# Kernel optimization log

Hardware: AMD Instinct MI355X
Metric: run time of the kernel (lower is better)

## Reference

```python
import jax, jax.numpy as jnp
import numpy as np

DIM = 256        # word / relation / entity-type embedding dim
STATEDIM = 256   # agent state dim
VOCAB = 100000
REL_COUNT = 25
T = 128          # sentence length


def _lstm(wvs, Wih, Whh, bih, bhh, reverse):
    # PyTorch LSTMCell gate order: i, f, g, o
    def step(carry, x):
        h, c = carry
        g = x @ Wih.T + bih + h @ Whh.T + bhh
        i, f, gg, o = jnp.split(g, 4)
        c = jax.nn.sigmoid(f) * c + jax.nn.sigmoid(i) * jnp.tanh(gg)
        h = jax.nn.sigmoid(o) * jnp.tanh(c)
        return (h, c), h
    init = (jnp.zeros((DIM,), jnp.float32), jnp.zeros((DIM,), jnp.float32))
    _, hs = jax.lax.scan(step, init, wvs, reverse=reverse)
    return hs


def setup_inputs() -> dict:
    key = jax.random.key(0)
    ks = jax.random.split(key, 32)
    def p(i, shape, scale=0.05):
        return (jax.random.normal(ks[i], shape) * scale).astype(jnp.float32)
    return {
        "text": jax.random.randint(ks[0], (T,), 0, VOCAB, dtype=jnp.int32),
        "wordvector": p(1, (VOCAB, DIM)),
        "relvec": p(2, (REL_COUNT + 1, DIM)),
        "entvec": p(3, (7, DIM)),
        "WihL": p(4, (4 * DIM, DIM)), "WhhL": p(5, (4 * DIM, DIM)),
        "bihL": p(6, (4 * DIM,)), "bhhL": p(7, (4 * DIM,)),
        "WihR": p(8, (4 * DIM, DIM)), "WhhR": p(9, (4 * DIM, DIM)),
        "bihR": p(10, (4 * DIM,)), "bhhR": p(11, (4 * DIM,)),
        "Wt": p(12, (STATEDIM, 3 * DIM + STATEDIM)), "bt": p(13, (STATEDIM,)),
        "Wp": p(14, (REL_COUNT + 1, STATEDIM)), "bp": p(15, (REL_COUNT + 1,)),
        "Wb": p(16, (STATEDIM, 3 * DIM + 2 * STATEDIM)), "bb": p(17, (STATEDIM,)),
        "Wpl": p(18, (REL_COUNT, 7, STATEDIM)), "bpl": p(19, (REL_COUNT, 7)),
        "Wtt": p(20, (STATEDIM, STATEDIM)), "btt": p(21, (STATEDIM,)),
        "Wtb": p(22, (STATEDIM, STATEDIM)), "btb": p(23, (STATEDIM,)),
        "Wbt": p(24, (STATEDIM, STATEDIM)), "bbt": p(25, (STATEDIM,)),
    }


def reference(text, wordvector, relvec, entvec, WihL, WhhL, bihL, bhhL,
              WihR, WhhR, bihR, bhhR, Wt, bt, Wp, bp, Wb, bb, Wpl, bpl,
              Wtt, btt, Wtb, btb, Wbt, bbt):
    # mode = "test_NER": deterministic argmax sampling, dropout disabled.
    wvs = wordvector[text]                               # [T, DIM]
    front = _lstm(wvs, WihL, WhhL, bihL, bhhL, False)    # [T, DIM]
    back = _lstm(wvs, WihR, WhhR, bihR, bhhR, True)      # [T, DIM]
    wordin = jnp.concatenate([front, back], axis=1)      # [T, 2*DIM]

    def bot_rollout(rel_idx, target, memb0):
        Wr, br = Wpl[rel_idx], bpl[rel_idx]              # per-relation head
        def stepb(carry, w):
            memb, ab = carry
            inpb = jnp.concatenate([w, entvec[ab], memb, target])
            outb = jnp.tanh(inpb @ Wb.T + bb)            # dropout off (test)
            probb = jax.nn.softmax(outb @ Wr.T + br)
            ab2 = jnp.argmax(probb).astype(jnp.int32)
            return (outb, ab2), (ab2, probb[ab2])
        (membf, _), (acts, aps) = jax.lax.scan(
            stepb, (memb0, jnp.zeros((), jnp.int32)), wordin)
        return membf, acts, aps

    def top_step(carry, w):
        mem, rel_action = carry
        inp = jnp.concatenate([w, relvec[rel_action], mem])
        outp = jnp.tanh(inp @ Wt.T + bt)                 # dropout off (test)
        prob = jax.nn.softmax(outp @ Wp.T + bp)
        action = jnp.argmax(prob).astype(jnp.int32)
        actprob = prob[action]
        do_ner = action > 0
        rel_next = jnp.where(do_ner, action, rel_action)
        rel_idx = jnp.maximum(action, 1) - 1
        target = outp @ Wtt.T + btt
        memb0 = outp @ Wtb.T + btb
        membf, acts, aps = bot_rollout(rel_idx, target, memb0)
        mem_after = membf @ Wbt.T + bbt
        mem_next = jnp.where(do_ner, mem_after, outp)
        acts = jnp.where(do_ner, acts, 0)
        aps = jnp.where(do_ner, aps, 0.0)
        return (mem_next, rel_next), (action, actprob, acts, aps)

    init = (jnp.zeros((STATEDIM,), jnp.float32), jnp.zeros((), jnp.int32))
    _, (top_actions, top_actprobs, bot_actions, bot_actprobs) = jax.lax.scan(
        top_step, init, wordin)
    # bot rows where no NER sub-rollout fired are zero-filled (orig: empty lists)
    return top_actions, top_actprobs, bot_actions, bot_actprobs
```

## Files before the change

kernel.cpp:

```cpp
#include <hip/hip_runtime.h>
#include <float.h>

constexpr int SEQ  = 128;
constexpr int D    = 256;
constexpr int G    = 1024;
constexpr int NREL = 26;
constexpr int NENT = 7;

typedef float v2f __attribute__((ext_vector_type(2)));

__global__ void k_trans(const float* __restrict__ in, float* __restrict__ out,
                        int rows, int cols, int in_stride, int in_off)
{
    int idx = blockIdx.x * 256 + threadIdx.x;
    if (idx >= rows * cols) return;
    int i = idx % rows;
    int k = idx / rows;
    out[idx] = in[(size_t)i * in_stride + in_off + k];
}

__global__ __launch_bounds__(1024) void k_xg(
    const int* __restrict__ text, const float* __restrict__ wv,
    const float* __restrict__ Wih, const float* __restrict__ bih,
    const float* __restrict__ bhh, float* __restrict__ xg)
{
    int t = blockIdx.x, j = threadIdx.x;
    const float* x  = wv + (size_t)text[t] * D;
    const float* wr = Wih + (size_t)j * D;
    float acc = bih[j] + bhh[j];
    for (int k = 0; k < D; ++k) acc += x[k] * wr[k];
    xg[t * G + j] = acc;
}

__global__ __launch_bounds__(1024) void k_lstm(
    const float* __restrict__ xgF, const float* __restrict__ xgB,
    const float* __restrict__ WHTF, const float* __restrict__ WHTB,
    float* __restrict__ wordin)
{
    int dir = blockIdx.x;
    const float* xg  = dir ? xgB  : xgF;
    const float* WHT = dir ? WHTB : WHTF;
    __shared__ float h[D], c[D], g[G];
    int j = threadIdx.x;
    if (j < D) { h[j] = 0.f; c[j] = 0.f; }
    __syncthreads();
    for (int s = 0; s < SEQ; ++s) {
        int t = dir ? (SEQ - 1 - s) : s;
        float acc = xg[t * G + j];
        for (int k = 0; k < D; ++k) acc += WHT[k * G + j] * h[k];
        g[j] = acc;
        __syncthreads();
        if (j < D) {
            float si = 1.f / (1.f + expf(-g[j]));
            float sf = 1.f / (1.f + expf(-g[D + j]));
            float gg = tanhf(g[2 * D + j]);
            float so = 1.f / (1.f + expf(-g[3 * D + j]));
            float cn = sf * c[j] + si * gg;
            float hn = so * tanhf(cn);
            c[j] = cn; h[j] = hn;
            wordin[t * (2 * D) + dir * D + j] = hn;
        }
        __syncthreads();
    }
}

__global__ __launch_bounds__(256) void k_prep2(
    const float* __restrict__ wordin,
    const float* __restrict__ WTWT, const float* __restrict__ WBWT,
    const float* __restrict__ WTRT, const float* __restrict__ WBET,
    const float* __restrict__ relvec, const float* __restrict__ entvec,
    const float* __restrict__ btv, const float* __restrict__ bbv,
    float* __restrict__ TW, float* __restrict__ BW,
    float* __restrict__ RV, float* __restrict__ EV)
{
    int b = blockIdx.x, i = threadIdx.x;
    if (b < SEQ) {
        const float* w = wordin + b * (2 * D);
        float a1 = btv[i], a2 = bbv[i];
        for (int j = 0; j < 2 * D; ++j) {
            float wv = w[j];
            a1 += wv * WTWT[j * D + i];
            a2 += wv * WBWT[j * D + i];
        }
        TW[b * D + i] = a1;
        BW[b * D + i] = a2;
    } else if (b < SEQ + NREL) {
        int r = b - SEQ;
        const float* x = relvec + r * D;
        float a = 0.f;
        for (int k = 0; k < D; ++k) a += x[k] * WTRT[k * D + i];
        RV[r * D + i] = a;
    } else {
        int e = b - SEQ - NREL;
        const float* x = entvec + e * D;
        float a = 0.f;
        for (int k = 0; k < D; ++k) a += x[k] * WBET[k * D + i];
        EV[e * D + i] = a;
    }
}

__global__ __launch_bounds__(256) void k_m1(
    const float* __restrict__ WBGT, const float* __restrict__ Wtt,
    float* __restrict__ M1T)
{
    int j = blockIdx.x, i = threadIdx.x;
    float a = 0.f;
    for (int k = 0; k < D; ++k) a = fmaf(WBGT[k * D + i], Wtt[k * D + j], a);
    M1T[j * D + i] = a;
}

__global__ __launch_bounds__(256) void k_c1(
    const float* __restrict__ WBGT, const float* __restrict__ btt,
    float* __restrict__ c1)
{
    int i = threadIdx.x;
    float a = 0.f;
    for (int k = 0; k < D; ++k) a = fmaf(WBGT[k * D + i], btt[k], a);
    c1[i] = a;
}

__global__ __launch_bounds__(256) void k_pack8r(
    const float* __restrict__ Wb, float* __restrict__ WREG)
{
    int e = blockIdx.x * 256 + threadIdx.x;
    int i = e >> 7, q = e & 127;
    WREG[e] = Wb[(size_t)i * (5 * D) + 3 * D + q];
}

__global__ __launch_bounds__(256) void k_pack8l(
    const float* __restrict__ Wb, float* __restrict__ WLDS)
{
    int f = blockIdx.x * 256 + threadIdx.x;
    int f4 = f >> 2, c = f & 3;
    int l = f4 & 63, rest = f4 >> 6;
    int j = rest % 24, w = rest / 24;
    WLDS[f] = Wb[(size_t)(w * 64 + l) * (5 * D) + 3 * D + 128 + 4 * j + c];
}

__global__ __launch_bounds__(256) void k_pack8g(
    const float* __restrict__ Wb, float* __restrict__ WGL)
{
    int f = blockIdx.x * 256 + threadIdx.x;
    int f4 = f >> 2, c = f & 3;
    int i = f4 & 255, j = f4 >> 8;
    WGL[f] = Wb[(size_t)i * (5 * D) + 3 * D + 224 + 4 * j + c];
}

__device__ inline float mv_full(const float* __restrict__ Wcol,
                                const float4* __restrict__ x4)
{
    float a0 = 0.f, a1 = 0.f, a2 = 0.f, a3 = 0.f;
    #pragma unroll 8
    for (int kk = 0; kk < 64; ++kk) {
        float4 xv = x4[kk];
        a0 = fmaf(Wcol[(4 * kk + 0) * D], xv.x, a0);
        a1 = fmaf(Wcol[(4 * kk + 1) * D], xv.y, a1);
        a2 = fmaf(Wcol[(4 * kk + 2) * D], xv.z, a2);
        a3 = fmaf(Wcol[(4 * kk + 3) * D], xv.w, a3);
    }
    return (a0 + a1) + (a2 + a3);
}

template<int W>
__device__ inline void grp_smax(float lv, int n, int lane, int& am, float& pm)
{
    float mx = lv;
    #pragma unroll
    for (int off = W / 2; off; off >>= 1) mx = fmaxf(mx, __shfl_xor(mx, off));
    float e  = (lane < n) ? expf(lv - mx) : 0.f;
    float se = e;
    #pragma unroll
    for (int off = W / 2; off; off >>= 1) se += __shfl_xor(se, off);
    float p  = (lane < n) ? (e / se) : -1.f;
    float q  = p;
    #pragma unroll
    for (int off = W / 2; off; off >>= 1) q = fmaxf(q, __shfl_xor(q, off));
    unsigned long long mask = __ballot(p == q);
    am = __ffsll((long long)mask) - 1;
    pm = q;
}

#define FMA_AB(Wv, Xv)                                                        \
    { float4 xx_ = (Xv);                                                      \
      A0 = __builtin_elementwise_fma((v2f){(Wv).x, (Wv).y},                   \
                                     (v2f){xx_.x, xx_.y}, A0);                \
      A1 = __builtin_elementwise_fma((v2f){(Wv).z, (Wv).w},                   \
                                     (v2f){xx_.z, xx_.w}, A1); }
#define FMA_CD(Wv, Xv)                                                        \
    { float4 xx_ = (Xv);                                                      \
      A2 = __builtin_elementwise_fma((v2f){(Wv).x, (Wv).y},                   \
                                     (v2f){xx_.x, xx_.y}, A2);                \
      A3 = __builtin_elementwise_fma((v2f){(Wv).z, (Wv).w},                   \
                                     (v2f){xx_.z, xx_.w}, A3); }

__global__ __launch_bounds__(256)
void k_main7(
    const float* __restrict__ TW,   const float* __restrict__ BW,
    const float* __restrict__ RV,   const float* __restrict__ EV,
    const float* __restrict__ WTMT, const float* __restrict__ WTBT,
    const float* __restrict__ WBTT, const float* __restrict__ M1T,
    const float* __restrict__ c1v,  const float* __restrict__ WREG,
    const float* __restrict__ WLDS, const float* __restrict__ WGL,
    const float* __restrict__ Wp,   const float* __restrict__ bp,
    const float* __restrict__ Wpl,  const float* __restrict__ bpl,
    const float* __restrict__ btb,  const float* __restrict__ bbt,
    float* __restrict__ out)
{
    const int tid  = threadIdx.x;
    const int lane = tid & 63;
    const int w8   = tid >> 6;

    __shared__ __align__(16) float wlds[256 * 96];
    __shared__ __align__(16) float xbuf[2][D];
    __shared__ __align__(16) float mem[D], outv[D];
    __shared__ __align__(16) float Esh[NENT * D], WrSh[NENT * D];
    __shared__ float lpartT[4][32];
    __shared__ float lpartB[2][4][8];
    __shared__ float brSh[8];

    {
        const float4* g4 = reinterpret_cast<const float4*>(WLDS);
        float4* w4 = reinterpret_cast<float4*>(wlds);
        #pragma unroll
        for (int it = 0; it < 24; ++it) w4[tid + it * 256] = g4[tid + it * 256];
    }
    for (int k = tid; k < NENT * D; k += 256) Esh[k] = EV[k];
    mem[tid] = 0.f;

    const float4* r4 = reinterpret_cast<const float4*>(WREG) + tid * 32;
    float4 wr0 = r4[0],   wr1 = r4[1],   wr2 = r4[2],   wr3 = r4[3];
    float4 wr4 = r4[4],   wr5 = r4[5],   wr6 = r4[6],   wr7 = r4[7];
    float4 wr8 = r4[8],   wr9 = r4[9],   wr10 = r4[10], wr11 = r4[11];
    float4 wr12 = r4[12], wr13 = r4[13], wr14 = r4[14], wr15 = r4[15];
    float4 wr16 = r4[16], wr17 = r4[17], wr18 = r4[18], wr19 = r4[19];
    float4 wr20 = r4[20], wr21 = r4[21], wr22 = r4[22], wr23 = r4[23];
    float4 wr24 = r4[24], wr25 = r4[25], wr26 = r4[26], wr27 = r4[27];
    float4 wr28 = r4[28], wr29 = r4[29], wr30 = r4[30], wr31 = r4[31];

    __syncthreads();

    const float4* wbase =
        reinterpret_cast<const float4*>(wlds) + (size_t)w8 * (24 * 64) + lane;
    const float4* gl = reinterpret_cast<const float4*>(WGL) + tid;

    const float* WTMc = WTMT + tid;
    const float* WTBc = WTBT + tid;
    const float* WBTc = WBTT + tid;
    const float* M1c  = M1T  + tid;

    int rel = 0;

    for (int t = 0; t < SEQ; ++t) {
        float a = mv_full(WTMc, reinterpret_cast<const float4*>(mem));
        float outp = tanhf(a + TW[t * D + tid] + RV[rel * D + tid]);
        outv[tid] = outp;
        for (int r = 0; r < NREL; ++r) {
            float pp = outp * Wp[r * D + tid];
            #pragma unroll
            for (int off = 32; off; off >>= 1) pp += __shfl_xor(pp, off);
            if (lane == 0) lpartT[w8][r] = pp;
        }
        __syncthreads();
        float lv = -FLT_MAX;
        if (lane < NREL)
            lv = lpartT[0][lane] + lpartT[1][lane] + lpartT[2][lane] +
                 lpartT[3][lane] + bp[lane];
        int am; float pm;
        grp_smax<32>(lv, NREL, lane, am, pm);
        if (tid == 0) { out[t] = (float)am; out[SEQ + t] = pm; }
        const int action = am;

        if (action > 0) {
            rel = action;
            float bs = mv_full(WTBc, reinterpret_cast<const float4*>(outv));
            float cs = mv_full(M1c,  reinterpret_cast<const float4*>(outv));
            const size_t wb0 = (size_t)(action - 1) * NENT * D;
            for (int k = tid; k < NENT * D; k += 256) WrSh[k] = Wpl[wb0 + k];
            if (tid < NENT) brSh[tid] = bpl[(action - 1) * NENT + tid];
            float btm = cs + c1v[tid];
            xbuf[0][tid] = bs + btb[tid];
            float bwc = BW[tid];
            __syncthreads();

            int p = 0, ab = 0;
            for (int s = 0; s < SEQ; ++s) {
                const float4* xb = reinterpret_cast<const float4*>(xbuf[p]);
                const float4* glv = gl;
                asm volatile("" : "+v"(glv));
                float4 g0 = glv[0 * 256], g1 = glv[1 * 256],
                       g2 = glv[2 * 256], g3 = glv[3 * 256],
                       g4 = glv[4 * 256], g5 = glv[5 * 256],
                       g6 = glv[6 * 256], g7 = glv[7 * 256];

                v2f A0 = {0.f, 0.f}, A1 = {0.f, 0.f},
                    A2 = {0.f, 0.f}, A3 = {0.f, 0.f};
                FMA_AB(wr0,  xb[0])  FMA_CD(wr1,  xb[1])
                FMA_AB(wr2,  xb[2])  FMA_CD(wr3,  xb[3])
                FMA_AB(wr4,  xb[4])  FMA_CD(wr5,  xb[5])
                FMA_AB(wr6,  xb[6])  FMA_CD(wr7,  xb[7])
                FMA_AB(wr8,  xb[8])  FMA_CD(wr9,  xb[9])
                FMA_AB(wr10, xb[10]) FMA_CD(wr11, xb[11])
                FMA_AB(wr12, xb[12]) FMA_CD(wr13, xb[13])
                FMA_AB(wr14, xb[14]) FMA_CD(wr15, xb[15])
                __builtin_amdgcn_sched_barrier(0);
                FMA_AB(wr16, xb[16]) FMA_CD(wr17, xb[17])
                FMA_AB(wr18, xb[18]) FMA_CD(wr19, xb[19])
                FMA_AB(wr20, xb[20]) FMA_CD(wr21, xb[21])
                FMA_AB(wr22, xb[22]) FMA_CD(wr23, xb[23])
                FMA_AB(wr24, xb[24]) FMA_CD(wr25, xb[25])
                FMA_AB(wr26, xb[26]) FMA_CD(wr27, xb[27])
                FMA_AB(wr28, xb[28]) FMA_CD(wr29, xb[29])
                FMA_AB(wr30, xb[30]) FMA_CD(wr31, xb[31])
                __builtin_amdgcn_sched_barrier(0);
                #pragma unroll
                for (int j = 0; j < 24; j += 8) {
                    float4 wa = wbase[(j + 0) * 64], wb_ = wbase[(j + 1) * 64];
                    float4 wc = wbase[(j + 2) * 64], wd  = wbase[(j + 3) * 64];
                    float4 we = wbase[(j + 4) * 64], wf  = wbase[(j + 5) * 64];
                    float4 wg = wbase[(j + 6) * 64], wh  = wbase[(j + 7) * 64];
                    FMA_AB(wa, xb[32 + j + 0]) FMA_CD(wb_, xb[32 + j + 1])
                    FMA_AB(wc, xb[32 + j + 2]) FMA_CD(wd,  xb[32 + j + 3])
                    FMA_AB(we, xb[32 + j + 4]) FMA_CD(wf,  xb[32 + j + 5])
                    FMA_AB(wg, xb[32 + j + 6]) FMA_CD(wh,  xb[32 + j + 7])
                    __builtin_amdgcn_sched_barrier(0);
                }
                FMA_AB(g0, xb[56]) FMA_CD(g1, xb[57])
                FMA_AB(g2, xb[58]) FMA_CD(g3, xb[59])
                FMA_AB(g4, xb[60]) FMA_CD(g5, xb[61])
                FMA_AB(g6, xb[62]) FMA_CD(g7, xb[63])
                v2f AS = (A0 + A1) + (A2 + A3);
                float ms = AS.x + AS.y;

                float ob = tanhf(ms + bwc + Esh[ab * D + tid] + btm);
                xbuf[p ^ 1][tid] = ob;
                #pragma unroll
                for (int r = 0; r < NENT; ++r) {
                    float pp = ob * WrSh[r * D + tid];
                    #pragma unroll
                    for (int off = 32; off; off >>= 1)
                        pp += __shfl_xor(pp, off);
                    if (lane == 0) lpartB[p][w8][r] = pp;
                }
                __syncthreads();
                float lv2 = -FLT_MAX;
                if (lane < NENT)
                    lv2 = lpartB[p][0][lane] + lpartB[p][1][lane] +
                          lpartB[p][2][lane] + lpartB[p][3][lane] + brSh[lane];
                int am2; float pm2;
                grp_smax<8>(lv2, NENT, lane, am2, pm2);
                if (tid == 0) {
                    out[2 * SEQ + t * SEQ + s] = (float)am2;
                    out[2 * SEQ + SEQ * SEQ + t * SEQ + s] = pm2;
                }
                ab = am2;
                int sn = (s + 1 < SEQ) ? s + 1 : s;
                bwc = BW[sn * D + tid];
                p ^= 1;
            }
            float es = mv_full(WBTc, reinterpret_cast<const float4*>(xbuf[p]));
            mem[tid] = es + bbt[tid];
            __syncthreads();
        } else {
            mem[tid] = outp;
            if (tid < SEQ) {
                out[2 * SEQ + t * SEQ + tid] = 0.f;
                out[2 * SEQ + SEQ * SEQ + t * SEQ + tid] = 0.f;
            }
            __syncthreads();
        }
    }
}

extern "C" void kernel_launch(void* const* d_in, const int* in_sizes, int n_in,
                              void* d_out, int out_size, void* d_ws, size_t ws_size,
                              hipStream_t stream)
{
    (void)in_sizes; (void)n_in; (void)out_size; (void)ws_size;
    const int*   text       = (const int*)  d_in[0];
    const float* wordvector = (const float*)d_in[1];
    const float* relvec     = (const float*)d_in[2];
    const float* entvec     = (const float*)d_in[3];
    const float* WihL = (const float*)d_in[4];  const float* WhhL = (const float*)d_in[5];
    const float* bihL = (const float*)d_in[6];  const float* bhhL = (const float*)d_in[7];
    const float* WihR = (const float*)d_in[8];  const float* WhhR = (const float*)d_in[9];
    const float* bihR = (const float*)d_in[10]; const float* bhhR = (const float*)d_in[11];
    const float* Wt   = (const float*)d_in[12]; const float* bt   = (const float*)d_in[13];
    const float* Wp   = (const float*)d_in[14]; const float* bp   = (const float*)d_in[15];
    const float* Wb   = (const float*)d_in[16]; const float* bb   = (const float*)d_in[17];
    const float* Wpl  = (const float*)d_in[18]; const float* bpl  = (const float*)d_in[19];
    const float* Wtt  = (const float*)d_in[20]; const float* btt  = (const float*)d_in[21];
    const float* Wtb  = (const float*)d_in[22]; const float* btb  = (const float*)d_in[23];
    const float* Wbt  = (const float*)d_in[24]; const float* bbt  = (const float*)d_in[25];

    float* ws = (float*)d_ws;
    size_t o = 0;
    auto take = [&](size_t n) { float* p = ws + o; o += n; return p; };
    float* XGF    = take(SEQ * G);
    float* XGB    = take(SEQ * G);
    float* WHLT   = take(D * G);
    float* WHRT   = take(D * G);
    float* WORDIN = take(SEQ * 2 * D);
    float* TW     = take(SEQ * D);
    float* BW     = take(SEQ * D);
    float* RVb    = take(NREL * D);
    float* EVb    = take(NENT * D);
    float* WTWT   = take(2 * D * D);
    float* WTRT   = take(D * D);
    float* WTMT   = take(D * D);
    float* WBWT   = take(2 * D * D);
    float* WBET   = take(D * D);
    float* WBGT   = take(D * D);
    float* WTBT   = take(D * D);
    float* WBTT   = take(D * D);
    float* M1T    = take(D * D);
    float* C1     = take(D);
    float* WREG   = take(256 * 128);
    float* WLDS   = take(256 * 96);
    float* WGL    = take(256 * 32);

    auto tr = [&](const float* in, float* outp, int rows, int cols, int stride, int off) {
        int n = rows * cols;
        k_trans<<<(n + 255) / 256, 256, 0, stream>>>(in, outp, rows, cols, stride, off);
    };
    tr(WhhL, WHLT, G, D, D, 0);
    tr(WhhR, WHRT, G, D, D, 0);
    tr(Wt,  WTWT, D, 2 * D, G, 0);
    tr(Wt,  WTRT, D, D, G, 512);
    tr(Wt,  WTMT, D, D, G, 768);
    tr(Wb,  WBWT, D, 2 * D, 5 * D, 0);
    tr(Wb,  WBET, D, D, 5 * D, 512);
    tr(Wb,  WBGT, D, D, 5 * D, 1024);
    tr(Wtb, WTBT, D, D, D, 0);
    tr(Wbt, WBTT, D, D, D, 0);

    k_m1<<<D, D, 0, stream>>>(WBGT, Wtt, M1T);
    k_c1<<<1, D, 0, stream>>>(WBGT, btt, C1);
    k_pack8r<<<128, 256, 0, stream>>>(Wb, WREG);
    k_pack8l<<<96, 256, 0, stream>>>(Wb, WLDS);
    k_pack8g<<<32, 256, 0, stream>>>(Wb, WGL);

    k_xg<<<SEQ, 1024, 0, stream>>>(text, wordvector, WihL, bihL, bhhL, XGF);
    k_xg<<<SEQ, 1024, 0, stream>>>(text, wordvector, WihR, bihR, bhhR, XGB);
    k_lstm<<<2, 1024, 0, stream>>>(XGF, XGB, WHLT, WHRT, WORDIN);
    k_prep2<<<SEQ + NREL + NENT, 256, 0, stream>>>(WORDIN, WTWT, WBWT, WTRT, WBET,
                                                   relvec, entvec, bt, bb,
                                                   TW, BW, RVb, EVb);
    k_main7<<<1, 256, 0, stream>>>(TW, BW, RVb, EVb, WTMT, WTBT, WBTT, M1T, C1,
                                   WREG, WLDS, WGL, Wp, bp, Wpl, bpl, btb, bbt,
                                   (float*)d_out);
}
```

Measured before the change: 66.93 ms.

## Rebalance bottom-recurrence weight split across registers, LDS and global memory

Changes how the 256-column bottom recurrent weight matrix is divided. Fewer columns are held in registers (48 instead of 128), more sit in shared memory (144 instead of 96) and more stream from global memory (64 instead of 32). The global loads are now interleaved in batches between LDS chunks so their latency overlaps with FMAs. The entity-vector table moves from shared memory into per-thread registers selected with a conditional chain, and the kernel is pinned to one wave per EU. The intent is to lower register pressure and spread the matvec across memory tiers, at the cost of more LDS and global traffic per step on the serial critical path.

```diff
diff --git a/kernel.cpp b/kernel.cpp
--- a/kernel.cpp
+++ b/kernel.cpp
@@ -119,31 +119,34 @@
     c1[i] = a;
 }
 
-__global__ __launch_bounds__(256) void k_pack8r(
+__global__ __launch_bounds__(256) void k_pack9r(
     const float* __restrict__ Wb, float* __restrict__ WREG)
 {
     int e = blockIdx.x * 256 + threadIdx.x;
-    int i = e >> 7, q = e & 127;
+    if (e >= 256 * 48) return;
+    int i = e / 48, q = e % 48;
     WREG[e] = Wb[(size_t)i * (5 * D) + 3 * D + q];
 }
 
-__global__ __launch_bounds__(256) void k_pack8l(
+__global__ __launch_bounds__(256) void k_pack9l(
     const float* __restrict__ Wb, float* __restrict__ WLDS)
 {
     int f = blockIdx.x * 256 + threadIdx.x;
+    if (f >= 256 * 144) return;
     int f4 = f >> 2, c = f & 3;
     int l = f4 & 63, rest = f4 >> 6;
-    int j = rest % 24, w = rest / 24;
-    WLDS[f] = Wb[(size_t)(w * 64 + l) * (5 * D) + 3 * D + 128 + 4 * j + c];
-}
-
-__global__ __launch_bounds__(256) void k_pack8g(
+    int j = rest % 36, w = rest / 36;
+    WLDS[f] = Wb[(size_t)(w * 64 + l) * (5 * D) + 3 * D + 48 + 4 * j + c];
+}
+
+__global__ __launch_bounds__(256) void k_pack9g(
     const float* __restrict__ Wb, float* __restrict__ WGL)
 {
     int f = blockIdx.x * 256 + threadIdx.x;
+    if (f >= 256 * 64) return;
     int f4 = f >> 2, c = f & 3;
     int i = f4 & 255, j = f4 >> 8;
-    WGL[f] = Wb[(size_t)i * (5 * D) + 3 * D + 224 + 4 * j + c];
+    WGL[f] = Wb[(size_t)i * (5 * D) + 3 * D + 192 + 4 * j + c];
 }
 
 __device__ inline float mv_full(const float* __restrict__ Wcol,
@@ -193,8 +196,25 @@
       A3 = __builtin_elementwise_fma((v2f){(Wv).z, (Wv).w},                   \
                                      (v2f){xx_.z, xx_.w}, A3); }
 
+#define LDS_CHUNK(c)                                                          \
+    { float4 la = wbase[(4 * (c) + 0) * 64], lb = wbase[(4 * (c) + 1) * 64],  \
+             lc = wbase[(4 * (c) + 2) * 64], ld = wbase[(4 * (c) + 3) * 64];  \
+      FMA_AB(la, xb[12 + 4 * (c) + 0]) FMA_CD(lb, xb[12 + 4 * (c) + 1])       \
+      FMA_AB(lc, xb[12 + 4 * (c) + 2]) FMA_CD(ld, xb[12 + 4 * (c) + 3])       \
+      __builtin_amdgcn_sched_barrier(0); }
+
+#define GBATCH(b)                                                             \
+    ga = glv[(4 * (b) + 0) * 256]; gb = glv[(4 * (b) + 1) * 256];             \
+    gc = glv[(4 * (b) + 2) * 256]; gd = glv[(4 * (b) + 3) * 256];
+
+#define GFMA(b)                                                               \
+    FMA_AB(ga, xb[48 + 4 * (b) + 0]) FMA_CD(gb, xb[48 + 4 * (b) + 1])         \
+    FMA_AB(gc, xb[48 + 4 * (b) + 2]) FMA_CD(gd, xb[48 + 4 * (b) + 3])         \
+    __builtin_amdgcn_sched_barrier(0);
+
 __global__ __launch_bounds__(256)
-void k_main7(
+__attribute__((amdgpu_waves_per_eu(1)))
+void k_main8(
     const float* __restrict__ TW,   const float* __restrict__ BW,
     const float* __restrict__ RV,   const float* __restrict__ EV,
     const float* __restrict__ WTMT, const float* __restrict__ WTBT,
@@ -210,10 +230,10 @@
     const int lane = tid & 63;
     const int w8   = tid >> 6;
 
-    __shared__ __align__(16) float wlds[256 * 96];
+    __shared__ __align__(16) float wlds[256 * 144];
     __shared__ __align__(16) float xbuf[2][D];
     __shared__ __align__(16) float mem[D], outv[D];
-    __shared__ __align__(16) float Esh[NENT * D], WrSh[NENT * D];
+    __shared__ __align__(16) float WrSh[NENT * D];
     __shared__ float lpartT[4][32];
     __shared__ float lpartB[2][4][8];
     __shared__ float brSh[8];
@@ -222,25 +242,23 @@
         const float4* g4 = reinterpret_cast<const float4*>(WLDS);
         float4* w4 = reinterpret_cast<float4*>(wlds);
         #pragma unroll
-        for (int it = 0; it < 24; ++it) w4[tid + it * 256] = g4[tid + it * 256];
+        for (int it = 0; it < 36; ++it) w4[tid + it * 256] = g4[tid + it * 256];
     }
-    for (int k = tid; k < NENT * D; k += 256) Esh[k] = EV[k];
     mem[tid] = 0.f;
 
-    const float4* r4 = reinterpret_cast<const float4*>(WREG) + tid * 32;
-    float4 wr0 = r4[0],   wr1 = r4[1],   wr2 = r4[2],   wr3 = r4[3];
-    float4 wr4 = r4[4],   wr5 = r4[5],   wr6 = r4[6],   wr7 = r4[7];
-    float4 wr8 = r4[8],   wr9 = r4[9],   wr10 = r4[10], wr11 = r4[11];
-    float4 wr12 = r4[12], wr13 = r4[13], wr14 = r4[14], wr15 = r4[15];
-    float4 wr16 = r4[16], wr17 = r4[17], wr18 = r4[18], wr19 = r4[19];
-    float4 wr20 = r4[20], wr21 = r4[21], wr22 = r4[22], wr23 = r4[23];
-    float4 wr24 = r4[24], wr25 = r4[25], wr26 = r4[26], wr27 = r4[27];
-    float4 wr28 = r4[28], wr29 = r4[29], wr30 = r4[30], wr31 = r4[31];
+    const float4* r4 = reinterpret_cast<const float4*>(WREG) + tid * 12;
+    float4 wr0 = r4[0],  wr1 = r4[1],  wr2 = r4[2],  wr3 = r4[3];
+    float4 wr4 = r4[4],  wr5 = r4[5],  wr6 = r4[6],  wr7 = r4[7];
+    float4 wr8 = r4[8],  wr9 = r4[9],  wr10 = r4[10], wr11 = r4[11];
+
+    float ev0 = EV[0 * D + tid], ev1 = EV[1 * D + tid], ev2 = EV[2 * D + tid],
+          ev3 = EV[3 * D + tid], ev4 = EV[4 * D + tid], ev5 = EV[5 * D + tid],
+          ev6 = EV[6 * D + tid];
 
     __syncthreads();
 
     const float4* wbase =
-        reinterpret_cast<const float4*>(wlds) + (size_t)w8 * (24 * 64) + lane;
+        reinterpret_cast<const float4*>(wlds) + (size_t)w8 * (36 * 64) + lane;
     const float4* gl = reinterpret_cast<const float4*>(WGL) + tid;
 
     const float* WTMc = WTMT + tid;
@@ -287,51 +305,39 @@
                 const float4* xb = reinterpret_cast<const float4*>(xbuf[p]);
                 const float4* glv = gl;
                 asm volatile("" : "+v"(glv));
-                float4 g0 = glv[0 * 256], g1 = glv[1 * 256],
-                       g2 = glv[2 * 256], g3 = glv[3 * 256],
-                       g4 = glv[4 * 256], g5 = glv[5 * 256],
-                       g6 = glv[6 * 256], g7 = glv[7 * 256];
 
                 v2f A0 = {0.f, 0.f}, A1 = {0.f, 0.f},
                     A2 = {0.f, 0.f}, A3 = {0.f, 0.f};
-                FMA_AB(wr0,  xb[0])  FMA_CD(wr1,  xb[1])
-                FMA_AB(wr2,  xb[2])  FMA_CD(wr3,  xb[3])
-                FMA_AB(wr4,  xb[4])  FMA_CD(wr5,  xb[5])
-                FMA_AB(wr6,  xb[6])  FMA_CD(wr7,  xb[7])
-                FMA_AB(wr8,  xb[8])  FMA_CD(wr9,  xb[9])
+                float4 ga, gb, gc, gd;
+                FMA_AB(wr0, xb[0]) FMA_CD(wr1, xb[1])
+                FMA_AB(wr2, xb[2]) FMA_CD(wr3, xb[3])
+                __builtin_amdgcn_sched_barrier(0);
+                FMA_AB(wr4, xb[4]) FMA_CD(wr5, xb[5])
+                FMA_AB(wr6, xb[6]) FMA_CD(wr7, xb[7])
+                __builtin_amdgcn_sched_barrier(0);
+                FMA_AB(wr8, xb[8])  FMA_CD(wr9, xb[9])
                 FMA_AB(wr10, xb[10]) FMA_CD(wr11, xb[11])
-                FMA_AB(wr12, xb[12]) FMA_CD(wr13, xb[13])
-                FMA_AB(wr14, xb[14]) FMA_CD(wr15, xb[15])
                 __builtin_amdgcn_sched_barrier(0);
-                FMA_AB(wr16, xb[16]) FMA_CD(wr17, xb[17])
-                FMA_AB(wr18, xb[18]) FMA_CD(wr19, xb[19])
-                FMA_AB(wr20, xb[20]) FMA_CD(wr21, xb[21])
-                FMA_AB(wr22, xb[22]) FMA_CD(wr23, xb[23])
-                FMA_AB(wr24, xb[24]) FMA_CD(wr25, xb[25])
-                FMA_AB(wr26, xb[26]) FMA_CD(wr27, xb[27])
-                FMA_AB(wr28, xb[28]) FMA_CD(wr29, xb[29])
-                FMA_AB(wr30, xb[30]) FMA_CD(wr31, xb[31])
-                __builtin_amdgcn_sched_barrier(0);
-                #pragma unroll
-                for (int j = 0; j < 24; j += 8) {
-                    float4 wa = wbase[(j + 0) * 64], wb_ = wbase[(j + 1) * 64];
-                    float4 wc = wbase[(j + 2) * 64], wd  = wbase[(j + 3) * 64];
-                    float4 we = wbase[(j + 4) * 64], wf  = wbase[(j + 5) * 64];
-                    float4 wg = wbase[(j + 6) * 64], wh  = wbase[(j + 7) * 64];
-                    FMA_AB(wa, xb[32 + j + 0]) FMA_CD(wb_, xb[32 + j + 1])
-                    FMA_AB(wc, xb[32 + j + 2]) FMA_CD(wd,  xb[32 + j + 3])
-                    FMA_AB(we, xb[32 + j + 4]) FMA_CD(wf,  xb[32 + j + 5])
-                    FMA_AB(wg, xb[32 + j + 6]) FMA_CD(wh,  xb[32 + j + 7])
-                    __builtin_amdgcn_sched_barrier(0);
-                }
-                FMA_AB(g0, xb[56]) FMA_CD(g1, xb[57])
-                FMA_AB(g2, xb[58]) FMA_CD(g3, xb[59])
-                FMA_AB(g4, xb[60]) FMA_CD(g5, xb[61])
-                FMA_AB(g6, xb[62]) FMA_CD(g7, xb[63])
+                GBATCH(0)
+                LDS_CHUNK(0) LDS_CHUNK(1)
+                GFMA(0)
+                GBATCH(1)
+                LDS_CHUNK(2) LDS_CHUNK(3)
+                GFMA(1)
+                GBATCH(2)
+                LDS_CHUNK(4) LDS_CHUNK(5)
+                GFMA(2)
+                GBATCH(3)
+                LDS_CHUNK(6) LDS_CHUNK(7)
+                GFMA(3)
+                LDS_CHUNK(8)
                 v2f AS = (A0 + A1) + (A2 + A3);
                 float ms = AS.x + AS.y;
 
-                float ob = tanhf(ms + bwc + Esh[ab * D + tid] + btm);
+                float ev = (ab == 0) ? ev0 : (ab == 1) ? ev1 :
+                           (ab == 2) ? ev2 : (ab == 3) ? ev3 :
+                           (ab == 4) ? ev4 : (ab == 5) ? ev5 : ev6;
+                float ob = tanhf(ms + bwc + ev + btm);
                 xbuf[p ^ 1][tid] = ob;
                 #pragma unroll
                 for (int r = 0; r < NENT; ++r) {
@@ -414,9 +420,9 @@
     float* WBTT   = take(D * D);
     float* M1T    = take(D * D);
     float* C1     = take(D);
-    float* WREG   = take(256 * 128);
-    float* WLDS   = take(256 * 96);
-    float* WGL    = take(256 * 32);
+    float* WREG   = take(256 * 48);
+    float* WLDS   = take(256 * 144);
+    float* WGL    = take(256 * 64);
 
     auto tr = [&](const float* in, float* outp, int rows, int cols, int stride, int off) {
         int n = rows * cols;
@@ -435,9 +441,9 @@
 
     k_m1<<<D, D, 0, stream>>>(WBGT, Wtt, M1T);
     k_c1<<<1, D, 0, stream>>>(WBGT, btt, C1);
-    k_pack8r<<<128, 256, 0, stream>>>(Wb, WREG);
-    k_pack8l<<<96, 256, 0, stream>>>(Wb, WLDS);
-    k_pack8g<<<32, 256, 0, stream>>>(Wb, WGL);
+    k_pack9r<<<48, 256, 0, stream>>>(Wb, WREG);
+    k_pack9l<<<144, 256, 0, stream>>>(Wb, WLDS);
+    k_pack9g<<<64, 256, 0, stream>>>(Wb, WGL);
 
     k_xg<<<SEQ, 1024, 0, stream>>>(text, wordvector, WihL, bihL, bhhL, XGF);
     k_xg<<<SEQ, 1024, 0, stream>>>(text, wordvector, WihR, bihR, bhhR, XGB);
@@ -445,7 +451,7 @@
     k_prep2<<<SEQ + NREL + NENT, 256, 0, stream>>>(WORDIN, WTWT, WBWT, WTRT, WBET,
                                                    relvec, entvec, bt, bb,
                                                    TW, BW, RVb, EVb);
-    k_main7<<<1, 256, 0, stream>>>(TW, BW, RVb, EVb, WTMT, WTBT, WBTT, M1T, C1,
+    k_main8<<<1, 256, 0, stream>>>(TW, BW, RVb, EVb, WTMT, WTBT, WBTT, M1T, C1,
                                    WREG, WLDS, WGL, Wp, bp, Wpl, bpl, btb, bbt,
                                    (float*)d_out);
 }
```

Result: slower. 85.61 ms (+27.9%).
